# Kernel tuning notes

Measured on AMD Instinct MI355X. Metric: run time of the kernel, lower is better.

Reference implementation:

```python
import jax, jax.numpy as jnp
import numpy as np

NENTITY = 200000
NRELATION = 500
HIDDEN = 256
GAMMA = 12.0
EPS = 2.0
EMB_RANGE = (GAMMA + EPS) / HIDDEN


def setup_inputs() -> dict:
    key = jax.random.key(0)
    ks = jax.random.split(key, 8)
    B, NEG = 256, 1024
    head = jax.random.randint(ks[0], (B, 1), 0, NENTITY)
    tail = jax.random.randint(ks[1], (B, NEG), 0, NENTITY)
    relation = jax.random.randint(ks[2], (B,), 0, NRELATION)
    entity_emb = jax.random.uniform(ks[3], (NENTITY, HIDDEN), jnp.float32, -EMB_RANGE, EMB_RANGE)
    relation_emb = jax.random.uniform(ks[4], (NRELATION, 2 * HIDDEN), jnp.float32, -EMB_RANGE, EMB_RANGE)
    lim = 1.0 / np.sqrt(2 * HIDDEN)
    W_fc = jax.random.uniform(ks[5], (HIDDEN, 2 * HIDDEN), jnp.float32, -lim, lim)
    b_fc = jax.random.uniform(ks[6], (HIDDEN,), jnp.float32, -lim, lim)
    return {"head": head, "tail": tail, "relation": relation,
            "entity_emb": entity_emb, "relation_emb": relation_emb,
            "W_fc": W_fc, "b_fc": b_fc}


def _l2_normalize(x):
    # F.normalize(x, p=2, dim=-1): x / max(||x||_2, 1e-12)
    n = jnp.sqrt(jnp.sum(x * x, axis=-1, keepdims=True))
    return x / jnp.maximum(n, 1e-12)


def reference(head, tail, relation, entity_emb, relation_emb, W_fc, b_fc):
    # gather embeddings
    h = entity_emb[head]                      # [B, 1,   d]
    t = entity_emb[tail]                      # [B, NEG, d]
    r = relation_emb[relation][:, None, :]    # [B, 1, 2d]
    re_head, re_tail = jnp.split(r, 2, axis=-1)   # each [B, 1, d]
    # broadcast relation halves to match head/tail sample counts, then concat
    re_h = jnp.broadcast_to(re_head, h.shape)
    re_t = jnp.broadcast_to(re_tail, t.shape)
    h_cat = jnp.concatenate([h, re_h], axis=-1)   # [B, 1,   2d]
    t_cat = jnp.concatenate([t, re_t], axis=-1)   # [B, NEG, 2d]
    # shared small FC (torch Linear: x @ W^T + b)
    h_fc = jnp.einsum('bnk,dk->bnd', h_cat, W_fc) + b_fc
    t_fc = jnp.einsum('bnk,dk->bnd', t_cat, W_fc) + b_fc
    h_n = _l2_normalize(h_fc)
    t_n = _l2_normalize(t_fc)
    diff = h_n - t_n                              # [B, NEG, d]
    score = GAMMA - jnp.sum(jnp.abs(diff), axis=2)  # [B, NEG]
    return score
```

## Files before the change

kernel.cpp:

```cpp
#include <hip/hip_runtime.h>
#include <hip/hip_bf16.h>
#include <math.h>

#define HIDDEN 256
#define NEG 1024
#define NBATCH 256
#define GAMMA_F 12.0f
#define BM 64
#define LDA 264
#define LDB 40

typedef short v8s __attribute__((ext_vector_type(8)));
typedef float v4f __attribute__((ext_vector_type(4)));

__device__ __forceinline__ short f2bf(float x) {
    unsigned int u = __float_as_uint(x);
    u = (u + 0x7fffu + ((u >> 16) & 1u)) >> 16;
    return (short)u;
}

__global__ __launch_bounds__(256) void prep_kernel(
    const int* __restrict__ head, const int* __restrict__ relation,
    const float* __restrict__ entity_emb, const float* __restrict__ relation_emb,
    const float* __restrict__ W_fc, const float* __restrict__ b_fc,
    short* __restrict__ W1bf, float* __restrict__ h_n, float* __restrict__ rel_part)
{
    const int b = blockIdx.x;
    const int t = threadIdx.x;

    W1bf[b * HIDDEN + t] = f2bf(W_fc[(size_t)b * 2 * HIDDEN + t]);

    __shared__ float xh[2 * HIDDEN];
    __shared__ float xt[HIDDEN];
    __shared__ float red[256];

    const int hidx = head[b];
    const int r = relation[b];
    xh[t]          = entity_emb[(size_t)hidx * HIDDEN + t];
    xh[HIDDEN + t] = relation_emb[(size_t)r * 2 * HIDDEN + t];
    xt[t]          = relation_emb[(size_t)r * 2 * HIDDEN + HIDDEN + t];
    __syncthreads();

    const float4* wrow = reinterpret_cast<const float4*>(W_fc + (size_t)t * 2 * HIDDEN);
    float hf = b_fc[t];
    float rp = b_fc[t];
    #pragma unroll 4
    for (int kk = 0; kk < HIDDEN / 4; ++kk) {
        float4 w = wrow[kk];
        hf += xh[4*kk+0]*w.x + xh[4*kk+1]*w.y + xh[4*kk+2]*w.z + xh[4*kk+3]*w.w;
    }
    #pragma unroll 4
    for (int kk = 0; kk < HIDDEN / 4; ++kk) {
        float4 w = wrow[HIDDEN/4 + kk];
        hf += xh[HIDDEN+4*kk+0]*w.x + xh[HIDDEN+4*kk+1]*w.y + xh[HIDDEN+4*kk+2]*w.z + xh[HIDDEN+4*kk+3]*w.w;
        rp += xt[4*kk+0]*w.x + xt[4*kk+1]*w.y + xt[4*kk+2]*w.z + xt[4*kk+3]*w.w;
    }
    rel_part[b * HIDDEN + t] = rp;

    red[t] = hf * hf;
    __syncthreads();
    for (int s = 128; s > 0; s >>= 1) {
        if (t < s) red[t] += red[t + s];
        __syncthreads();
    }
    const float norm = sqrtf(red[0]);
    h_n[b * HIDDEN + t] = hf / fmaxf(norm, 1e-12f);
}

__global__ __launch_bounds__(256) void score_kernel(
    const int* __restrict__ tail, const float* __restrict__ entity_emb,
    const short* __restrict__ W1bf, const float* __restrict__ h_n,
    const float* __restrict__ rel_part, float* __restrict__ out)
{
    __shared__ __align__(16) short As[BM * LDA];
    __shared__ __align__(16) short Bs[HIDDEN * LDB];

    const int t = threadIdx.x;
    const int m0 = blockIdx.x * BM;
    const int b = m0 >> 10;

    {
        const int rl = t >> 2;
        const int q  = t & 3;
        const int erow = tail[m0 + rl];
        const float4* s4 = reinterpret_cast<const float4*>(
            entity_emb + (size_t)erow * HIDDEN + q * 64);
        short* dst = As + rl * LDA + q * 64;
        #pragma unroll
        for (int it = 0; it < 8; ++it) {
            float4 a0 = s4[it*2], a1 = s4[it*2+1];
            v8s v;
            v[0]=f2bf(a0.x); v[1]=f2bf(a0.y); v[2]=f2bf(a0.z); v[3]=f2bf(a0.w);
            v[4]=f2bf(a1.x); v[5]=f2bf(a1.y); v[6]=f2bf(a1.z); v[7]=f2bf(a1.w);
            *reinterpret_cast<v8s*>(dst + it*8) = v;
        }
    }

    const int w    = t >> 6;
    const int lane = t & 63;
    const int g    = lane >> 4;
    const int c    = lane & 15;

    v4f acc[16];
    #pragma unroll
    for (int i = 0; i < 16; ++i) acc[i] = v4f{0.f, 0.f, 0.f, 0.f};

    const short* a_base = As + (16 * w + c) * LDA + g * 8;
    const short* b_base = Bs + c * LDB + g * 8;

    for (int kt = 0; kt < 8; ++kt) {
        __syncthreads();
        {
            const int chunk = t & 3;
            const int nrow  = t >> 2;
            const short* wsrc = W1bf + kt * 32 + chunk * 8;
            #pragma unroll
            for (int i = 0; i < 4; ++i) {
                const int n = nrow + 64 * i;
                v8s v = *reinterpret_cast<const v8s*>(wsrc + (size_t)n * HIDDEN);
                *reinterpret_cast<v8s*>(Bs + n * LDB + chunk * 8) = v;
            }
        }
        __syncthreads();
        v8s a = *reinterpret_cast<const v8s*>(a_base + kt * 32);
        #pragma unroll
        for (int nt = 0; nt < 16; ++nt) {
            v8s bf = *reinterpret_cast<const v8s*>(b_base + nt * 16 * LDB);
            acc[nt] = __builtin_amdgcn_mfma_f32_16x16x32_bf16(a, bf, acc[nt], 0, 0, 0);
        }
    }

    float hnv[16], rlv[16];
    #pragma unroll
    for (int nt = 0; nt < 16; ++nt) {
        const int d = nt * 16 + c;
        hnv[nt] = h_n[b * HIDDEN + d];
        rlv[nt] = rel_part[b * HIDDEN + d];
    }
    float sc4[4];
    #pragma unroll
    for (int reg = 0; reg < 4; ++reg) {
        float tf[16];
        float ssq = 0.f;
        #pragma unroll
        for (int nt = 0; nt < 16; ++nt) {
            tf[nt] = acc[nt][reg] + rlv[nt];
            ssq += tf[nt] * tf[nt];
        }
        #pragma unroll
        for (int mask = 1; mask < 16; mask <<= 1) ssq += __shfl_xor(ssq, mask);
        const float rn = 1.f / fmaxf(sqrtf(ssq), 1e-12f);
        float s = 0.f;
        #pragma unroll
        for (int nt = 0; nt < 16; ++nt) s += fabsf(hnv[nt] - tf[nt] * rn);
        #pragma unroll
        for (int mask = 1; mask < 16; mask <<= 1) s += __shfl_xor(s, mask);
        sc4[reg] = GAMMA_F - s;
    }
    if (c == 0) {
        float4 o = make_float4(sc4[0], sc4[1], sc4[2], sc4[3]);
        *reinterpret_cast<float4*>(out + m0 + 16 * w + 4 * g) = o;
    }
}

extern "C" void kernel_launch(void* const* d_in, const int* in_sizes, int n_in,
                              void* d_out, int out_size, void* d_ws, size_t ws_size,
                              hipStream_t stream)
{
    const int*   head         = (const int*)d_in[0];
    const int*   tail         = (const int*)d_in[1];
    const int*   relation     = (const int*)d_in[2];
    const float* entity_emb   = (const float*)d_in[3];
    const float* relation_emb = (const float*)d_in[4];
    const float* W_fc         = (const float*)d_in[5];
    const float* b_fc         = (const float*)d_in[6];
    float* out = (float*)d_out;

    short* W1bf     = (short*)d_ws;
    float* h_n      = (float*)((char*)d_ws + 131072);
    float* rel_part = (float*)((char*)d_ws + 131072 + 262144);

    prep_kernel<<<NBATCH, 256, 0, stream>>>(head, relation, entity_emb, relation_emb,
                                            W_fc, b_fc, W1bf, h_n, rel_part);
    score_kernel<<<(NBATCH * NEG) / BM, 256, 0, stream>>>(tail, entity_emb, W1bf,
                                                          h_n, rel_part, out);
}
```

Baseline: 369.7 us.

## Hold W fragments in registers and split N across waves in score kernel

The score kernel is reorganized so that each wave owns 64 output columns and keeps its bf16 W fragments in registers, loaded directly from global memory. This removes the per-k-step LDS staging of W and its barriers. The A tile is written to LDS in MFMA-fragment order without padding, so each wave now runs 4x4 MFMA tiles over all 64 rows. Row norms and L1 sums are reduced across waves through small LDS arrays, which adds two barriers and raises register pressure. The kernel also declares a 2-blocks-per-CU occupancy hint.

```diff
diff --git a/kernel.cpp b/kernel.cpp
--- a/kernel.cpp
+++ b/kernel.cpp
@@ -1,5 +1,4 @@
 #include <hip/hip_runtime.h>
-#include <hip/hip_bf16.h>
 #include <math.h>
 
 #define HIDDEN 256
@@ -7,8 +6,6 @@
 #define NBATCH 256
 #define GAMMA_F 12.0f
 #define BM 64
-#define LDA 264
-#define LDB 40
 
 typedef short v8s __attribute__((ext_vector_type(8)));
 typedef float v4f __attribute__((ext_vector_type(4)));
@@ -67,99 +64,137 @@
     h_n[b * HIDDEN + t] = hf / fmaxf(norm, 1e-12f);
 }
 
-__global__ __launch_bounds__(256) void score_kernel(
+__global__ __launch_bounds__(256, 2) void score_kernel(
     const int* __restrict__ tail, const float* __restrict__ entity_emb,
     const short* __restrict__ W1bf, const float* __restrict__ h_n,
     const float* __restrict__ rel_part, float* __restrict__ out)
 {
-    __shared__ __align__(16) short As[BM * LDA];
-    __shared__ __align__(16) short Bs[HIDDEN * LDB];
-
-    const int t = threadIdx.x;
+    __shared__ __align__(16) short As[BM * HIDDEN];
+    __shared__ float ssq_lds[4][BM];
+    __shared__ float l1_lds[4][BM];
+
+    const int t  = threadIdx.x;
     const int m0 = blockIdx.x * BM;
-    const int b = m0 >> 10;
-
-    {
-        const int rl = t >> 2;
-        const int q  = t & 3;
-        const int erow = tail[m0 + rl];
-        const float4* s4 = reinterpret_cast<const float4*>(
-            entity_emb + (size_t)erow * HIDDEN + q * 64);
-        short* dst = As + rl * LDA + q * 64;
-        #pragma unroll
-        for (int it = 0; it < 8; ++it) {
-            float4 a0 = s4[it*2], a1 = s4[it*2+1];
-            v8s v;
-            v[0]=f2bf(a0.x); v[1]=f2bf(a0.y); v[2]=f2bf(a0.z); v[3]=f2bf(a0.w);
-            v[4]=f2bf(a1.x); v[5]=f2bf(a1.y); v[6]=f2bf(a1.z); v[7]=f2bf(a1.w);
-            *reinterpret_cast<v8s*>(dst + it*8) = v;
-        }
-    }
-
-    const int w    = t >> 6;
-    const int lane = t & 63;
-    const int g    = lane >> 4;
-    const int c    = lane & 15;
-
-    v4f acc[16];
-    #pragma unroll
-    for (int i = 0; i < 16; ++i) acc[i] = v4f{0.f, 0.f, 0.f, 0.f};
-
-    const short* a_base = As + (16 * w + c) * LDA + g * 8;
-    const short* b_base = Bs + c * LDB + g * 8;
-
+    const int b  = blockIdx.x >> 4;
+
+    const int c = t & 15;
+    const int g = (t >> 4) & 3;
+    const int w = t >> 6;
+    const int l = t & 63;
+
+    int rows[4];
+    #pragma unroll
+    for (int mt = 0; mt < 4; ++mt) rows[mt] = tail[m0 + mt * 16 + c];
+
+    #pragma unroll
+    for (int i = 0; i < 8; ++i) {
+        const int s  = w + 4 * i;
+        const int kt = s & 7;
+        const int mt = s >> 3;
+        const float4* src = reinterpret_cast<const float4*>(
+            entity_emb + (size_t)rows[mt] * HIDDEN + (kt * 4 + g) * 8);
+        float4 a0 = src[0], a1 = src[1];
+        v8s v;
+        v[0]=f2bf(a0.x); v[1]=f2bf(a0.y); v[2]=f2bf(a0.z); v[3]=f2bf(a0.w);
+        v[4]=f2bf(a1.x); v[5]=f2bf(a1.y); v[6]=f2bf(a1.z); v[7]=f2bf(a1.w);
+        *reinterpret_cast<v8s*>(As + (t + 256 * i) * 8) = v;
+    }
+
+    v8s Bf[4][8];
+    #pragma unroll
+    for (int ntl = 0; ntl < 4; ++ntl) {
+        const short* bsrc = W1bf + (size_t)(64 * w + ntl * 16 + c) * HIDDEN + g * 8;
+        #pragma unroll
+        for (int kt = 0; kt < 8; ++kt)
+            Bf[ntl][kt] = *reinterpret_cast<const v8s*>(bsrc + kt * 32);
+    }
+
+    v4f acc[4][4];
+    #pragma unroll
+    for (int mt = 0; mt < 4; ++mt)
+        #pragma unroll
+        for (int ntl = 0; ntl < 4; ++ntl)
+            acc[mt][ntl] = v4f{0.f, 0.f, 0.f, 0.f};
+
+    __syncthreads();
+
+    #pragma unroll
     for (int kt = 0; kt < 8; ++kt) {
-        __syncthreads();
-        {
-            const int chunk = t & 3;
-            const int nrow  = t >> 2;
-            const short* wsrc = W1bf + kt * 32 + chunk * 8;
-            #pragma unroll
-            for (int i = 0; i < 4; ++i) {
-                const int n = nrow + 64 * i;
-                v8s v = *reinterpret_cast<const v8s*>(wsrc + (size_t)n * HIDDEN);
-                *reinterpret_cast<v8s*>(Bs + n * LDB + chunk * 8) = v;
+        v8s a[4];
+        #pragma unroll
+        for (int mt = 0; mt < 4; ++mt)
+            a[mt] = *reinterpret_cast<const v8s*>(As + (mt * 512 + kt * 64 + l) * 8);
+        #pragma unroll
+        for (int mt = 0; mt < 4; ++mt) {
+            #pragma unroll
+            for (int ntl = 0; ntl < 4; ++ntl)
+                acc[mt][ntl] = __builtin_amdgcn_mfma_f32_16x16x32_bf16(
+                    a[mt], Bf[ntl][kt], acc[mt][ntl], 0, 0, 0);
+        }
+    }
+
+    float rlv[4], hnv[4];
+    #pragma unroll
+    for (int ntl = 0; ntl < 4; ++ntl) {
+        const int n = 64 * w + ntl * 16 + c;
+        rlv[ntl] = rel_part[b * HIDDEN + n];
+        hnv[ntl] = h_n[b * HIDDEN + n];
+    }
+
+    #pragma unroll
+    for (int mt = 0; mt < 4; ++mt) {
+        float ssq[4] = {0.f, 0.f, 0.f, 0.f};
+        #pragma unroll
+        for (int ntl = 0; ntl < 4; ++ntl) {
+            #pragma unroll
+            for (int r = 0; r < 4; ++r) {
+                float tf = acc[mt][ntl][r] + rlv[ntl];
+                acc[mt][ntl][r] = tf;
+                ssq[r] += tf * tf;
             }
         }
-        __syncthreads();
-        v8s a = *reinterpret_cast<const v8s*>(a_base + kt * 32);
-        #pragma unroll
-        for (int nt = 0; nt < 16; ++nt) {
-            v8s bf = *reinterpret_cast<const v8s*>(b_base + nt * 16 * LDB);
-            acc[nt] = __builtin_amdgcn_mfma_f32_16x16x32_bf16(a, bf, acc[nt], 0, 0, 0);
-        }
-    }
-
-    float hnv[16], rlv[16];
-    #pragma unroll
-    for (int nt = 0; nt < 16; ++nt) {
-        const int d = nt * 16 + c;
-        hnv[nt] = h_n[b * HIDDEN + d];
-        rlv[nt] = rel_part[b * HIDDEN + d];
-    }
-    float sc4[4];
-    #pragma unroll
-    for (int reg = 0; reg < 4; ++reg) {
-        float tf[16];
-        float ssq = 0.f;
-        #pragma unroll
-        for (int nt = 0; nt < 16; ++nt) {
-            tf[nt] = acc[nt][reg] + rlv[nt];
-            ssq += tf[nt] * tf[nt];
-        }
-        #pragma unroll
-        for (int mask = 1; mask < 16; mask <<= 1) ssq += __shfl_xor(ssq, mask);
-        const float rn = 1.f / fmaxf(sqrtf(ssq), 1e-12f);
-        float s = 0.f;
-        #pragma unroll
-        for (int nt = 0; nt < 16; ++nt) s += fabsf(hnv[nt] - tf[nt] * rn);
-        #pragma unroll
-        for (int mask = 1; mask < 16; mask <<= 1) s += __shfl_xor(s, mask);
-        sc4[reg] = GAMMA_F - s;
-    }
-    if (c == 0) {
-        float4 o = make_float4(sc4[0], sc4[1], sc4[2], sc4[3]);
-        *reinterpret_cast<float4*>(out + m0 + 16 * w + 4 * g) = o;
+        #pragma unroll
+        for (int mask = 1; mask < 16; mask <<= 1) {
+            #pragma unroll
+            for (int r = 0; r < 4; ++r) ssq[r] += __shfl_xor(ssq[r], mask);
+        }
+        if (c == 0) {
+            #pragma unroll
+            for (int r = 0; r < 4; ++r) ssq_lds[w][mt * 16 + g * 4 + r] = ssq[r];
+        }
+    }
+    __syncthreads();
+
+    #pragma unroll
+    for (int mt = 0; mt < 4; ++mt) {
+        float rn[4], s1[4] = {0.f, 0.f, 0.f, 0.f};
+        #pragma unroll
+        for (int r = 0; r < 4; ++r) {
+            const int m = mt * 16 + g * 4 + r;
+            float tot = ssq_lds[0][m] + ssq_lds[1][m] + ssq_lds[2][m] + ssq_lds[3][m];
+            rn[r] = 1.f / fmaxf(sqrtf(tot), 1e-12f);
+        }
+        #pragma unroll
+        for (int ntl = 0; ntl < 4; ++ntl) {
+            #pragma unroll
+            for (int r = 0; r < 4; ++r)
+                s1[r] += fabsf(hnv[ntl] - acc[mt][ntl][r] * rn[r]);
+        }
+        #pragma unroll
+        for (int mask = 1; mask < 16; mask <<= 1) {
+            #pragma unroll
+            for (int r = 0; r < 4; ++r) s1[r] += __shfl_xor(s1[r], mask);
+        }
+        if (c == 0) {
+            #pragma unroll
+            for (int r = 0; r < 4; ++r) l1_lds[w][mt * 16 + g * 4 + r] = s1[r];
+        }
+    }
+    __syncthreads();
+
+    if (t < BM) {
+        out[m0 + t] = GAMMA_F -
+            (l1_lds[0][t] + l1_lds[1][t] + l1_lds[2][t] + l1_lds[3][t]);
     }
 }
 
```

Measured after the change: 367.1 us. No clear change (-0.7%).

## Make score kernel persistent with resident W tile and register-prefetched gathers

Applied to the files above, without the earlier changes.

The score kernel becomes persistent: 256 blocks of 512 threads load the full bf16 W slice into LDS once, and each wave processes 128 rows in 8 iterations. Gathered embedding rows are read straight into registers as A fragments, and the next row group is prefetched while MFMAs run on the current one, so the As staging buffer and the per-k-tile W reloads and barriers go away. Float-to-bf16 packing now uses perm-based round-half-up instead of round-to-nearest-even, which changes rounding slightly. The epilogue batches the shuffle reductions across the four accumulator rows. In exchange, register pressure rises (16 float4 prefetch registers plus 16 accumulators), and grid-level parallelism drops to one large block per CU.

```diff
diff --git a/kernel.cpp b/kernel.cpp
--- a/kernel.cpp
+++ b/kernel.cpp
@@ -1,22 +1,31 @@
 #include <hip/hip_runtime.h>
-#include <hip/hip_bf16.h>
 #include <math.h>
 
 #define HIDDEN 256
 #define NEG 1024
 #define NBATCH 256
 #define GAMMA_F 12.0f
-#define BM 64
-#define LDA 264
-#define LDB 40
+#define LDB 264
+#define NBLK 256
 
 typedef short v8s __attribute__((ext_vector_type(8)));
 typedef float v4f __attribute__((ext_vector_type(4)));
+typedef unsigned int u32;
 
 __device__ __forceinline__ short f2bf(float x) {
-    unsigned int u = __float_as_uint(x);
+    u32 u = __float_as_uint(x);
     u = (u + 0x7fffu + ((u >> 16) & 1u)) >> 16;
     return (short)u;
+}
+
+__device__ __forceinline__ u32 rhu(float f) { return __float_as_uint(f) + 0x8000u; }
+__device__ __forceinline__ v8s pack8(const float4& x0, const float4& x1) {
+    int4 fr;
+    fr.x = __builtin_amdgcn_perm(rhu(x0.y), rhu(x0.x), 0x07060302u);
+    fr.y = __builtin_amdgcn_perm(rhu(x0.w), rhu(x0.z), 0x07060302u);
+    fr.z = __builtin_amdgcn_perm(rhu(x1.y), rhu(x1.x), 0x07060302u);
+    fr.w = __builtin_amdgcn_perm(rhu(x1.w), rhu(x1.z), 0x07060302u);
+    return __builtin_bit_cast(v8s, fr);
 }
 
 __global__ __launch_bounds__(256) void prep_kernel(
@@ -67,99 +76,115 @@
     h_n[b * HIDDEN + t] = hf / fmaxf(norm, 1e-12f);
 }
 
-__global__ __launch_bounds__(256) void score_kernel(
+__global__ __launch_bounds__(512, 2) void score_kernel(
     const int* __restrict__ tail, const float* __restrict__ entity_emb,
     const short* __restrict__ W1bf, const float* __restrict__ h_n,
     const float* __restrict__ rel_part, float* __restrict__ out)
 {
-    __shared__ __align__(16) short As[BM * LDA];
     __shared__ __align__(16) short Bs[HIDDEN * LDB];
 
     const int t = threadIdx.x;
-    const int m0 = blockIdx.x * BM;
-    const int b = m0 >> 10;
+    const int w = t >> 6;
+    const int c = t & 15;
+    const int g = (t >> 4) & 3;
 
     {
-        const int rl = t >> 2;
-        const int q  = t & 3;
-        const int erow = tail[m0 + rl];
-        const float4* s4 = reinterpret_cast<const float4*>(
-            entity_emb + (size_t)erow * HIDDEN + q * 64);
-        short* dst = As + rl * LDA + q * 64;
-        #pragma unroll
-        for (int it = 0; it < 8; ++it) {
-            float4 a0 = s4[it*2], a1 = s4[it*2+1];
-            v8s v;
-            v[0]=f2bf(a0.x); v[1]=f2bf(a0.y); v[2]=f2bf(a0.z); v[3]=f2bf(a0.w);
-            v[4]=f2bf(a1.x); v[5]=f2bf(a1.y); v[6]=f2bf(a1.z); v[7]=f2bf(a1.w);
-            *reinterpret_cast<v8s*>(dst + it*8) = v;
-        }
-    }
-
-    const int w    = t >> 6;
-    const int lane = t & 63;
-    const int g    = lane >> 4;
-    const int c    = lane & 15;
-
-    v4f acc[16];
-    #pragma unroll
-    for (int i = 0; i < 16; ++i) acc[i] = v4f{0.f, 0.f, 0.f, 0.f};
-
-    const short* a_base = As + (16 * w + c) * LDA + g * 8;
-    const short* b_base = Bs + c * LDB + g * 8;
-
-    for (int kt = 0; kt < 8; ++kt) {
-        __syncthreads();
-        {
-            const int chunk = t & 3;
-            const int nrow  = t >> 2;
-            const short* wsrc = W1bf + kt * 32 + chunk * 8;
-            #pragma unroll
-            for (int i = 0; i < 4; ++i) {
-                const int n = nrow + 64 * i;
-                v8s v = *reinterpret_cast<const v8s*>(wsrc + (size_t)n * HIDDEN);
-                *reinterpret_cast<v8s*>(Bs + n * LDB + chunk * 8) = v;
-            }
-        }
-        __syncthreads();
-        v8s a = *reinterpret_cast<const v8s*>(a_base + kt * 32);
-        #pragma unroll
-        for (int nt = 0; nt < 16; ++nt) {
-            v8s bf = *reinterpret_cast<const v8s*>(b_base + nt * 16 * LDB);
-            acc[nt] = __builtin_amdgcn_mfma_f32_16x16x32_bf16(a, bf, acc[nt], 0, 0, 0);
-        }
-    }
-
-    float hnv[16], rlv[16];
+        const int n = t >> 1;
+        const int h = (t & 1) * 128;
+        const short* src = W1bf + (size_t)n * HIDDEN + h;
+        short* dst = Bs + n * LDB + h;
+        #pragma unroll
+        for (int i = 0; i < 16; ++i)
+            *reinterpret_cast<v8s*>(dst + i * 8) = *reinterpret_cast<const v8s*>(src + i * 8);
+    }
+
+    const int m0w = (blockIdx.x * 8 + w) * 128;
+    const int b   = m0w >> 10;
+
+    float rlv[16], hnv[16];
     #pragma unroll
     for (int nt = 0; nt < 16; ++nt) {
-        const int d = nt * 16 + c;
-        hnv[nt] = h_n[b * HIDDEN + d];
-        rlv[nt] = rel_part[b * HIDDEN + d];
-    }
-    float sc4[4];
+        rlv[nt] = rel_part[b * HIDDEN + nt * 16 + c];
+        hnv[nt] = h_n[b * HIDDEN + nt * 16 + c];
+    }
+
+    int rows[8];
     #pragma unroll
-    for (int reg = 0; reg < 4; ++reg) {
-        float tf[16];
-        float ssq = 0.f;
-        #pragma unroll
-        for (int nt = 0; nt < 16; ++nt) {
-            tf[nt] = acc[nt][reg] + rlv[nt];
-            ssq += tf[nt] * tf[nt];
-        }
-        #pragma unroll
-        for (int mask = 1; mask < 16; mask <<= 1) ssq += __shfl_xor(ssq, mask);
-        const float rn = 1.f / fmaxf(sqrtf(ssq), 1e-12f);
-        float s = 0.f;
-        #pragma unroll
-        for (int nt = 0; nt < 16; ++nt) s += fabsf(hnv[nt] - tf[nt] * rn);
-        #pragma unroll
-        for (int mask = 1; mask < 16; mask <<= 1) s += __shfl_xor(s, mask);
-        sc4[reg] = GAMMA_F - s;
-    }
-    if (c == 0) {
-        float4 o = make_float4(sc4[0], sc4[1], sc4[2], sc4[3]);
-        *reinterpret_cast<float4*>(out + m0 + 16 * w + 4 * g) = o;
+    for (int j = 0; j < 8; ++j) rows[j] = tail[m0w + j * 16 + c];
+
+    float4 ld[16];
+    {
+        const float* p = entity_emb + (size_t)rows[0] * HIDDEN + g * 8;
+        #pragma unroll
+        for (int kt = 0; kt < 8; ++kt) {
+            ld[2 * kt]     = *reinterpret_cast<const float4*>(p + kt * 32);
+            ld[2 * kt + 1] = *reinterpret_cast<const float4*>(p + kt * 32 + 4);
+        }
+    }
+
+    __syncthreads();
+
+    #pragma unroll 1
+    for (int j = 0; j < 8; ++j) {
+        const float* pn = entity_emb + (size_t)rows[(j + 1) & 7] * HIDDEN + g * 8;
+
+        v4f acc[16];
+        #pragma unroll
+        for (int nt = 0; nt < 16; ++nt) acc[nt] = v4f{0.f, 0.f, 0.f, 0.f};
+
+        #pragma unroll
+        for (int kt = 0; kt < 8; ++kt) {
+            float4 x0 = ld[2 * kt], x1 = ld[2 * kt + 1];
+            if (j != 7) {
+                ld[2 * kt]     = *reinterpret_cast<const float4*>(pn + kt * 32);
+                ld[2 * kt + 1] = *reinterpret_cast<const float4*>(pn + kt * 32 + 4);
+            }
+            v8s a = pack8(x0, x1);
+            #pragma unroll
+            for (int nt = 0; nt < 16; ++nt) {
+                v8s bf = *reinterpret_cast<const v8s*>(
+                    Bs + (nt * 16 + c) * LDB + kt * 32 + g * 8);
+                acc[nt] = __builtin_amdgcn_mfma_f32_16x16x32_bf16(a, bf, acc[nt], 0, 0, 0);
+            }
+        }
+
+        float sc4[4];
+        {
+            float ssq[4] = {0.f, 0.f, 0.f, 0.f};
+            #pragma unroll
+            for (int nt = 0; nt < 16; ++nt) {
+                #pragma unroll
+                for (int r = 0; r < 4; ++r) {
+                    float tf = acc[nt][r] + rlv[nt];
+                    acc[nt][r] = tf;
+                    ssq[r] += tf * tf;
+                }
+            }
+            #pragma unroll
+            for (int mask = 1; mask < 16; mask <<= 1) {
+                #pragma unroll
+                for (int r = 0; r < 4; ++r) ssq[r] += __shfl_xor(ssq[r], mask);
+            }
+            #pragma unroll
+            for (int r = 0; r < 4; ++r) {
+                float rn = 1.f / fmaxf(sqrtf(ssq[r]), 1e-12f);
+                float s = 0.f;
+                #pragma unroll
+                for (int nt = 0; nt < 16; ++nt)
+                    s += fabsf(hnv[nt] - acc[nt][r] * rn);
+                sc4[r] = s;
+            }
+            #pragma unroll
+            for (int mask = 1; mask < 16; mask <<= 1) {
+                #pragma unroll
+                for (int r = 0; r < 4; ++r) sc4[r] += __shfl_xor(sc4[r], mask);
+            }
+        }
+        if (c == 0) {
+            float4 o = make_float4(GAMMA_F - sc4[0], GAMMA_F - sc4[1],
+                                   GAMMA_F - sc4[2], GAMMA_F - sc4[3]);
+            *reinterpret_cast<float4*>(out + m0w + j * 16 + g * 4) = o;
+        }
     }
 }
 
@@ -182,6 +207,6 @@
 
     prep_kernel<<<NBATCH, 256, 0, stream>>>(head, relation, entity_emb, relation_emb,
                                             W_fc, b_fc, W1bf, h_n, rel_part);
-    score_kernel<<<(NBATCH * NEG) / BM, 256, 0, stream>>>(tail, entity_emb, W1bf,
-                                                          h_n, rel_part, out);
-}
+    score_kernel<<<NBLK, 512, 0, stream>>>(tail, entity_emb, W1bf,
+                                           h_n, rel_part, out);
+}
```

Result: slower. 919.6 us (+148.7%).
